# Kernel tuning notes

Measured on AMD Instinct MI355X. Metric: run time of the kernel, lower is better.

The kernel has to match this reference:

```python
import jax, jax.numpy as jnp
import numpy as np
from jax import lax

NUM_CLASSES = 21
KSIZE = 11
DIL = 1
BLUR = 4
NUM_STEPS = 5
YX_SCALE = 80.0
RGB_SCALE = 13.0
POS_SCALE = 3.0


def _ceil_pad_factor(sizes, factor):
    offs = tuple((factor - s % factor) % factor for s in sizes)
    return tuple((o + 1) // 2 for o in offs)


def avg_pool_nopad(x, k, pad):
    # F.avg_pool2d(kernel=stride=k, padding=pad, count_include_pad=False)
    pcfg = ((0, 0), (0, 0), (pad[0], pad[0]), (pad[1], pad[1]))
    s = lax.reduce_window(x, jnp.float32(0), lax.add, (1, 1, k, k), (1, 1, k, k), pcfg)
    ones = jnp.ones((1, 1) + x.shape[2:], x.dtype)
    cnt = lax.reduce_window(ones, jnp.float32(0), lax.add, (1, 1, k, k), (1, 1, k, k), pcfg)
    return s / cnt


def _patches(x, k, dil):
    # im2col with zero padding (matches torch F.unfold used by pac)
    pad = (k // 2) * dil
    p = lax.conv_general_dilated_patches(
        x, (k, k), (1, 1), [(pad, pad), (pad, pad)], rhs_dilation=(dil, dil))
    B, C, H, W = x.shape
    return p.reshape(B, C, k * k, H, W)


def gaussian_kernel(feat, k, dil):
    # pixel-adaptive Gaussian kernel: exp(-0.5 * ||f_i - f_j||^2) over the KxK window
    p = _patches(feat, k, dil)                       # [B,F,k2,H,W]
    d = p - feat[:, :, None]
    return jnp.exp(-0.5 * jnp.sum(d * d, axis=1))    # [B,k2,H,W]


def pac_message(Q, kernel, k, dil):
    # shared-filter (Potts, spatial_filter=False) pac conv: per-channel kernel-weighted sum
    p = _patches(Q, k, dil)                          # [B,C,k2,h,w]
    return jnp.einsum('bckhw,bkhw->bchw', p, kernel)


def upsample_bilinear(x, scale):
    # matches F.interpolate(mode='bilinear', align_corners=False)
    B, C, h, w = x.shape
    def idx_w(n_in):
        n_out = n_in * scale
        src = jnp.clip((jnp.arange(n_out, dtype=jnp.float32) + 0.5) / scale - 0.5, 0.0, n_in - 1.0)
        i0 = jnp.floor(src).astype(jnp.int32)
        i1 = jnp.minimum(i0 + 1, n_in - 1)
        return i0, i1, (src - i0).astype(x.dtype)
    y0, y1, wy = idx_w(h)
    x0, x1, wx = idx_w(w)
    xh = x[:, :, y0, :] * (1 - wy)[None, None, :, None] + x[:, :, y1, :] * wy[None, None, :, None]
    return xh[:, :, :, x0] * (1 - wx)[None, None, None, :] + xh[:, :, :, x1] * wx[None, None, None, :]


def crf_forward(x, w_backbone, b_backbone, unary_weight, pairwise_weights):
    B, _, H, W = x.shape
    # backbone stub: 3x3 conv producing unary logits [B,21,H,W]
    unary = lax.conv_general_dilated(
        x, w_backbone, (1, 1), [(1, 1), (1, 1)],
        dimension_numbers=('NCHW', 'OIHW', 'NCHW')) + b_backbone[None, :, None, None]
    # edge features: bilateral (YX/80, RGB/13) and spatial (YX/3)
    yx = jnp.stack(jnp.meshgrid(jnp.arange(H, dtype=x.dtype), jnp.arange(W, dtype=x.dtype), indexing='ij'))
    yx = jnp.broadcast_to(yx[None], (B, 2, H, W))
    feat_bilateral = jnp.concatenate([yx / YX_SCALE, x / RGB_SCALE], axis=1)  # [B,5,H,W]
    feat_spatial = yx / POS_SCALE                                             # [B,2,H,W]
    pad = _ceil_pad_factor((H, W), BLUR)
    kernels = [gaussian_kernel(avg_pool_nopad(f, BLUR, pad), KSIZE, DIL)
               for f in (feat_bilateral, feat_spatial)]

    def step(logQ, unary, k1, k2, uw, pw):
        Q = jax.nn.softmax(logQ, axis=1)
        Qb = avg_pool_nopad(Q, BLUR, pad)
        new = uw * unary
        for kern, w in ((k1, pw[0]), (k2, pw[1])):
            msg = pac_message(Qb, kern, KSIZE, DIL)
            msg = upsample_bilinear(msg, BLUR)[:, :, pad[0]:pad[0] + H, pad[1]:pad[1] + W]
            new = new + w * msg
        return new

    logQ = unary
    for _ in range(NUM_STEPS):
        logQ = step(logQ, unary, kernels[0], kernels[1], unary_weight, pairwise_weights)
    return logQ  # final_output == 'log_Q'


def setup_inputs():
    key = jax.random.key(0)
    ks = jax.random.split(key, 3)
    B, H, W = 2, 512, 512
    x = jax.random.uniform(ks[0], (B, 3, H, W), jnp.float32) * 255.0  # image in [0,255]
    w_backbone = jax.random.normal(ks[1], (NUM_CLASSES, 3, 3, 3), jnp.float32) * 0.1
    b_backbone = jax.random.normal(ks[2], (NUM_CLASSES,), jnp.float32) * 0.01
    unary_weight = jnp.asarray(0.8, jnp.float32)
    pairwise_weights = jnp.asarray([2.0, 0.6], jnp.float32)
    return {"x": x, "w_backbone": w_backbone, "b_backbone": b_backbone,
            "unary_weight": unary_weight, "pairwise_weights": pairwise_weights}


def reference(x, w_backbone, b_backbone, unary_weight, pairwise_weights):
    return crf_forward(x, w_backbone, b_backbone, unary_weight, pairwise_weights)
```

## Files before the change

### kernel.cpp

```cpp
#include <hip/hip_runtime.h>

#define NCH 21
#define HWP (1 << 14)
#define KS 11
#define KK 121
#define PTW 32
#define PTH 8
#define LROW 48
#define LHGT 18
#define LPLANE (LROW * LHGT)

__global__ __launch_bounds__(256) void k_conv_sm(const float* __restrict__ x,
                                                 const float* __restrict__ w,
                                                 const float* __restrict__ bias,
                                                 float* __restrict__ unary,
                                                 float* __restrict__ qb) {
    int idx = blockIdx.x * 256 + threadIdx.x;
    int r = idx & 3;
    int xqi = (idx >> 2) & 127;
    int py = (idx >> 9) & 127;
    int b = idx >> 16;
    int y = 4 * py + r;
    int xq = xqi << 2;

    float p[3][3][6];
#pragma unroll
    for (int ch = 0; ch < 3; ++ch) {
        const float* xp = x + (((size_t)(b * 3 + ch)) << 18);
#pragma unroll
        for (int rr = 0; rr < 3; ++rr) {
            int yy = y + rr - 1;
            if ((unsigned)yy >= 512u) {
#pragma unroll
                for (int j = 0; j < 6; ++j) p[ch][rr][j] = 0.f;
            } else {
                const float* row = xp + (yy << 9);
                float4 v = *(const float4*)(row + xq);
                p[ch][rr][1] = v.x; p[ch][rr][2] = v.y; p[ch][rr][3] = v.z; p[ch][rr][4] = v.w;
                p[ch][rr][0] = (xq > 0) ? row[xq - 1] : 0.f;
                p[ch][rr][5] = (xq + 4 < 512) ? row[xq + 4] : 0.f;
            }
        }
    }
    float a[NCH][4];
    for (int o = 0; o < NCH; ++o) {
        const float* wp = w + o * 27;
        float bz = bias[o];
        float a0 = bz, a1 = bz, a2 = bz, a3 = bz;
#pragma unroll
        for (int ch = 0; ch < 3; ++ch)
#pragma unroll
            for (int rr = 0; rr < 3; ++rr) {
                float w0 = wp[ch * 9 + rr * 3 + 0];
                float w1 = wp[ch * 9 + rr * 3 + 1];
                float w2 = wp[ch * 9 + rr * 3 + 2];
                const float* pr = p[ch][rr];
                a0 += w0 * pr[0] + w1 * pr[1] + w2 * pr[2];
                a1 += w0 * pr[1] + w1 * pr[2] + w2 * pr[3];
                a2 += w0 * pr[2] + w1 * pr[3] + w2 * pr[4];
                a3 += w0 * pr[3] + w1 * pr[4] + w2 * pr[5];
            }
        *(float4*)(unary + (((size_t)(b * NCH + o)) << 18) + (y << 9) + xq) =
            make_float4(a0, a1, a2, a3);
        a[o][0] = a0; a[o][1] = a1; a[o][2] = a2; a[o][3] = a3;
    }
    float qsum[NCH];
#pragma unroll
    for (int c = 0; c < NCH; ++c) qsum[c] = 0.f;
#pragma unroll
    for (int i2 = 0; i2 < 4; ++i2) {
        float m = a[0][i2];
#pragma unroll
        for (int c = 1; c < NCH; ++c) m = fmaxf(m, a[c][i2]);
        float s = 0.f;
#pragma unroll
        for (int c = 0; c < NCH; ++c) { float e = __expf(a[c][i2] - m); a[c][i2] = e; s += e; }
        float inv = 1.0f / s;
#pragma unroll
        for (int c = 0; c < NCH; ++c) qsum[c] += a[c][i2] * inv;
    }
#pragma unroll
    for (int c = 0; c < NCH; ++c) {
        float v = qsum[c];
        v += __shfl_xor(v, 1);
        v += __shfl_xor(v, 2);
        if (r == 0) qb[(((size_t)(b * NCH + c)) << 14) + (py << 7) + xqi] = v * 0.0625f;
    }
}

__global__ __launch_bounds__(256) void k_pool_rgb(const float* __restrict__ x,
                                                  float* __restrict__ prgb) {
    int idx = blockIdx.x * 256 + threadIdx.x;
    int p = idx & (HWP - 1);
    int ch = (idx >> 14) % 3;
    int b = idx / (3 * HWP);
    int py = p >> 7, px = p & 127;
    const float* xp = x + (((size_t)(b * 3 + ch)) << 18);
    float s = 0.f;
#pragma unroll
    for (int r = 0; r < 4; ++r) {
        const float4 v = *(const float4*)(xp + (((4 * py + r) << 9) + 4 * px));
        s += v.x + v.y + v.z + v.w;
    }
    prgb[idx] = s * 0.0625f;
}

__global__ __launch_bounds__(256) void k_build_kc(const float* __restrict__ prgb,
                                                  const float* __restrict__ pw,
                                                  float* __restrict__ kc) {
    int idx = blockIdx.x * 256 + threadIdx.x;
    int p = idx & (HWP - 1);
    int jj = idx >> 14;
    int b = (jj >= KK) ? 1 : 0;
    int j = jj - KK * b;
    int dy = j / KS, dx = j - dy * KS;
    int py = p >> 7, px = p & 127;
    float pw0 = pw[0], pw1 = pw[1];

    const float inv13 = 1.0f / 13.0f;
    float fy = (4.f * py + 1.5f) * (1.0f / 80.0f);
    float fx = (4.f * px + 1.5f) * (1.0f / 80.0f);
    const float* pb = prgb + (size_t)b * 3 * HWP;
    float r0 = pb[p] * inv13;
    float g0 = pb[HWP + p] * inv13;
    float b0 = pb[2 * HWP + p] * inv13;
    float sy = (4.f * py + 1.5f) * (1.0f / 3.0f);
    float sx = (4.f * px + 1.5f) * (1.0f / 3.0f);

    int ny = py + dy - 5;
    int nx = px + dx - 5;
    float s1, s2;
    if ((unsigned)ny < 128u && (unsigned)nx < 128u) {
        int np = (ny << 7) + nx;
        float r2 = pb[np] * inv13;
        float g2 = pb[HWP + np] * inv13;
        float b2 = pb[2 * HWP + np] * inv13;
        float dya = fy - (4.f * ny + 1.5f) * (1.0f / 80.0f);
        float dxa = fx - (4.f * nx + 1.5f) * (1.0f / 80.0f);
        float dr = r0 - r2, dg = g0 - g2, db = b0 - b2;
        s1 = dya * dya + dxa * dxa + dr * dr + dg * dg + db * db;
        float dys = sy - (4.f * ny + 1.5f) * (1.0f / 3.0f);
        float dxs = sx - (4.f * nx + 1.5f) * (1.0f / 3.0f);
        s2 = dys * dys + dxs * dxs;
    } else {
        s1 = fy * fy + fx * fx + r0 * r0 + g0 * g0 + b0 * b0;
        s2 = sy * sy + sx * sx;
    }
    kc[idx] = pw0 * __expf(-0.5f * s1) + pw1 * __expf(-0.5f * s2);
}

__global__ __launch_bounds__(256) void k_pac4(const float* __restrict__ qb,
                                              const float* __restrict__ kc,
                                              float* __restrict__ msgc) {
    int tile = blockIdx.x & 63;
    int cg = (blockIdx.x >> 6) % 6;
    int b = blockIdx.x / 384;
    int tx0 = (tile & 3) * PTW;
    int ty0 = (tile >> 2) * PTH;
    int c0 = cg * 4;

    __shared__ float lq[4 * LPLANE];

    const float* qbb = qb + (((size_t)(b * NCH)) << 14);
    for (int i = threadIdx.x; i < 4 * LPLANE; i += 256) {
        int c = i / LPLANE;
        int rem = i - c * LPLANE;
        int ly = rem / LROW;
        int lx = rem - ly * LROW;
        int ch = c0 + c;
        int gy = ty0 + ly - 5, gx = tx0 + lx - 5;
        float v = 0.f;
        if (ch < NCH && lx < 42 && (unsigned)gy < 128u && (unsigned)gx < 128u)
            v = qbb[((size_t)ch << 14) + (gy << 7) + gx];
        lq[i] = v;
    }
    __syncthreads();

    int s = threadIdx.x & 63;
    int cl = threadIdx.x >> 6;
    int my = s >> 3;
    int mx0 = (s & 7) << 2;
    int ch = c0 + cl;

    float acc0 = 0.f, acc1 = 0.f, acc2 = 0.f, acc3 = 0.f;
    int p0 = ((ty0 + my) << 7) + tx0 + mx0;
    const float* kcb = kc + (((size_t)(b * KK)) << 14) + p0;
    const float* lbase = lq + cl * LPLANE + mx0;

    for (int dy = 0; dy < KS; ++dy) {
        const float* lp = lbase + (my + dy) * LROW;
        float4 v0 = *(const float4*)(lp + 0);
        float4 v1 = *(const float4*)(lp + 4);
        float4 v2 = *(const float4*)(lp + 8);
        float4 v3 = *(const float4*)(lp + 12);
        float rb[16] = {v0.x, v0.y, v0.z, v0.w, v1.x, v1.y, v1.z, v1.w,
                        v2.x, v2.y, v2.z, v2.w, v3.x, v3.y, v3.z, v3.w};
        const float* kcrow = kcb + (((size_t)(dy * KS)) << 14);
#pragma unroll
        for (int dx = 0; dx < KS; ++dx) {
            float4 k4 = *(const float4*)(kcrow + (((size_t)dx) << 14));
            acc0 += k4.x * rb[dx + 0];
            acc1 += k4.y * rb[dx + 1];
            acc2 += k4.z * rb[dx + 2];
            acc3 += k4.w * rb[dx + 3];
        }
    }
    if (ch < NCH)
        *(float4*)(msgc + (((size_t)(b * NCH + ch)) << 14) + p0) =
            make_float4(acc0, acc1, acc2, acc3);
}

__global__ __launch_bounds__(256) void k_step(const float* __restrict__ unary,
                                              const float* __restrict__ msgc,
                                              const float* __restrict__ uwp,
                                              float* __restrict__ qb,
                                              float* __restrict__ out,
                                              int write_out) {
    int idx = blockIdx.x * 256 + threadIdx.x;
    int r = idx & 3;
    int px = (idx >> 2) & 127;
    int py = (idx >> 9) & 127;
    int b = idx >> 16;
    int y = 4 * py + r;
    float uw = uwp[0];

    int rA = (r < 2) ? max(py - 1, 0) : py;
    int rB = (r < 2) ? py : min(py + 1, 127);
    float fy = (r == 0) ? 0.625f : (r == 1) ? 0.875f : (r == 2) ? 0.125f : 0.375f;
    int xm1 = max(px - 1, 0), xp1 = min(px + 1, 127);
    int oA = rA << 7, oB = rB << 7;

    size_t base = (((size_t)(b * NCH)) << 18) + (y << 9) + (px << 2);
    const float* up = unary + base;
    const float* mp = msgc + (((size_t)(b * NCH)) << 14);

    float a[NCH][4];
#pragma unroll
    for (int c = 0; c < NCH; ++c) {
        float4 u4 = *(const float4*)(up + ((size_t)c << 18));
        const float* m0 = mp + ((size_t)c << 14);
        float aL = m0[oA + xm1], aM = m0[oA + px], aR = m0[oA + xp1];
        float bL = m0[oB + xm1], bM = m0[oB + px], bR = m0[oB + xp1];
        float cL = aL + (bL - aL) * fy;
        float cM = aM + (bM - aM) * fy;
        float cR = aR + (bR - aR) * fy;
        a[c][0] = uw * u4.x + cL + (cM - cL) * 0.625f;
        a[c][1] = uw * u4.y + cL + (cM - cL) * 0.875f;
        a[c][2] = uw * u4.z + cM + (cR - cM) * 0.125f;
        a[c][3] = uw * u4.w + cM + (cR - cM) * 0.375f;
    }

    if (write_out) {
        float* op = out + base;
#pragma unroll
        for (int c = 0; c < NCH; ++c)
            *(float4*)(op + ((size_t)c << 18)) = make_float4(a[c][0], a[c][1], a[c][2], a[c][3]);
        return;
    }

    float qsum[NCH];
#pragma unroll
    for (int c = 0; c < NCH; ++c) qsum[c] = 0.f;
#pragma unroll
    for (int i2 = 0; i2 < 4; ++i2) {
        float m = a[0][i2];
#pragma unroll
        for (int c = 1; c < NCH; ++c) m = fmaxf(m, a[c][i2]);
        float ss = 0.f;
#pragma unroll
        for (int c = 0; c < NCH; ++c) { float e = __expf(a[c][i2] - m); a[c][i2] = e; ss += e; }
        float inv = 1.0f / ss;
#pragma unroll
        for (int c = 0; c < NCH; ++c) qsum[c] += a[c][i2] * inv;
    }
#pragma unroll
    for (int c = 0; c < NCH; ++c) {
        float v = qsum[c];
        v += __shfl_xor(v, 1);
        v += __shfl_xor(v, 2);
        if (r == 0) qb[(((size_t)(b * NCH + c)) << 14) + (py << 7) + px] = v * 0.0625f;
    }
}

extern "C" void kernel_launch(void* const* d_in, const int* in_sizes, int n_in,
                              void* d_out, int out_size, void* d_ws, size_t ws_size,
                              hipStream_t stream) {
    const float* x  = (const float*)d_in[0];
    const float* wb = (const float*)d_in[1];
    const float* bb = (const float*)d_in[2];
    const float* uw = (const float*)d_in[3];
    const float* pw = (const float*)d_in[4];
    float* out = (float*)d_out;

    float* ws    = (float*)d_ws;
    float* unary = ws;
    float* kc    = unary + 11010048;
    float* qb    = kc + 3964928;
    float* msgc  = qb + 688128;
    float* prgb  = msgc;

    k_conv_sm<<<512, 256, 0, stream>>>(x, wb, bb, unary, qb);
    k_pool_rgb<<<384, 256, 0, stream>>>(x, prgb);
    k_build_kc<<<15488, 256, 0, stream>>>(prgb, pw, kc);

    for (int s = 0; s < 5; ++s) {
        k_pac4<<<768, 256, 0, stream>>>(qb, kc, msgc);
        k_step<<<512, 256, 0, stream>>>(unary, msgc, uw, qb, out, (s == 4) ? 1 : 0);
    }
}
```

Baseline: 284.0 us.

## Store PAC kernel weights in fp16 and stage message tile in LDS for step

The precomputed 121-tap Gaussian kernel is stored as half precision, which halves the bytes k_pac4 streams from global memory in each of the five iterations; accumulation stays in fp32. k_step is also reorganised so that each block handles half of one low-res row and first stages the needed three message rows (with clamped halo) into shared memory. The bilinear reads then come from LDS instead of scattered global loads. The cost is reduced kernel-weight precision, which may change outputs slightly, plus an extra barrier and LDS staging in k_step.

```diff
diff --git a/kernel.cpp b/kernel.cpp
--- a/kernel.cpp
+++ b/kernel.cpp
@@ -9,6 +9,8 @@
 #define LROW 48
 #define LHGT 18
 #define LPLANE (LROW * LHGT)
+
+typedef _Float16 half4 __attribute__((ext_vector_type(4)));
 
 __global__ __launch_bounds__(256) void k_conv_sm(const float* __restrict__ x,
                                                  const float* __restrict__ w,
@@ -107,7 +109,7 @@
 
 __global__ __launch_bounds__(256) void k_build_kc(const float* __restrict__ prgb,
                                                   const float* __restrict__ pw,
-                                                  float* __restrict__ kc) {
+                                                  _Float16* __restrict__ kc) {
     int idx = blockIdx.x * 256 + threadIdx.x;
     int p = idx & (HWP - 1);
     int jj = idx >> 14;
@@ -146,11 +148,11 @@
         s1 = fy * fy + fx * fx + r0 * r0 + g0 * g0 + b0 * b0;
         s2 = sy * sy + sx * sx;
     }
-    kc[idx] = pw0 * __expf(-0.5f * s1) + pw1 * __expf(-0.5f * s2);
+    kc[idx] = (_Float16)(pw0 * __expf(-0.5f * s1) + pw1 * __expf(-0.5f * s2));
 }
 
 __global__ __launch_bounds__(256) void k_pac4(const float* __restrict__ qb,
-                                              const float* __restrict__ kc,
+                                              const _Float16* __restrict__ kc,
                                               float* __restrict__ msgc) {
     int tile = blockIdx.x & 63;
     int cg = (blockIdx.x >> 6) % 6;
@@ -184,7 +186,7 @@
 
     float acc0 = 0.f, acc1 = 0.f, acc2 = 0.f, acc3 = 0.f;
     int p0 = ((ty0 + my) << 7) + tx0 + mx0;
-    const float* kcb = kc + (((size_t)(b * KK)) << 14) + p0;
+    const _Float16* kcb = kc + (((size_t)(b * KK)) << 14) + p0;
     const float* lbase = lq + cl * LPLANE + mx0;
 
     for (int dy = 0; dy < KS; ++dy) {
@@ -195,14 +197,14 @@
         float4 v3 = *(const float4*)(lp + 12);
         float rb[16] = {v0.x, v0.y, v0.z, v0.w, v1.x, v1.y, v1.z, v1.w,
                         v2.x, v2.y, v2.z, v2.w, v3.x, v3.y, v3.z, v3.w};
-        const float* kcrow = kcb + (((size_t)(dy * KS)) << 14);
+        const _Float16* kcrow = kcb + (((size_t)(dy * KS)) << 14);
 #pragma unroll
         for (int dx = 0; dx < KS; ++dx) {
-            float4 k4 = *(const float4*)(kcrow + (((size_t)dx) << 14));
-            acc0 += k4.x * rb[dx + 0];
-            acc1 += k4.y * rb[dx + 1];
-            acc2 += k4.z * rb[dx + 2];
-            acc3 += k4.w * rb[dx + 3];
+            half4 k4 = *(const half4*)(kcrow + (((size_t)dx) << 14));
+            acc0 += (float)k4.x * rb[dx + 0];
+            acc1 += (float)k4.y * rb[dx + 1];
+            acc2 += (float)k4.z * rb[dx + 2];
+            acc3 += (float)k4.w * rb[dx + 3];
         }
     }
     if (ch < NCH)
@@ -216,31 +218,46 @@
                                               float* __restrict__ qb,
                                               float* __restrict__ out,
                                               int write_out) {
-    int idx = blockIdx.x * 256 + threadIdx.x;
-    int r = idx & 3;
-    int px = (idx >> 2) & 127;
-    int py = (idx >> 9) & 127;
-    int b = idx >> 16;
+    int half = blockIdx.x & 1;
+    int py = (blockIdx.x >> 1) & 127;
+    int b = blockIdx.x >> 8;
+    int px0 = half << 6;
+
+    __shared__ float lmsg[NCH * 3 * 66];
+
+    const float* mbase = msgc + (((size_t)(b * NCH)) << 14);
+    for (int i = threadIdx.x; i < NCH * 198; i += 256) {
+        int c = i / 198;
+        int rem = i - c * 198;
+        int row = rem / 66;
+        int j = rem - row * 66;
+        int ry = min(max(py - 1 + row, 0), 127);
+        int gx = min(max(px0 - 1 + j, 0), 127);
+        lmsg[i] = mbase[((size_t)c << 14) + (ry << 7) + gx];
+    }
+    __syncthreads();
+
+    int r = threadIdx.x & 3;
+    int lpx = threadIdx.x >> 2;
+    int px = px0 + lpx;
     int y = 4 * py + r;
     float uw = uwp[0];
 
-    int rA = (r < 2) ? max(py - 1, 0) : py;
-    int rB = (r < 2) ? py : min(py + 1, 127);
+    int iA = (r < 2) ? 0 : 1;
+    int iB = iA + 1;
     float fy = (r == 0) ? 0.625f : (r == 1) ? 0.875f : (r == 2) ? 0.125f : 0.375f;
-    int xm1 = max(px - 1, 0), xp1 = min(px + 1, 127);
-    int oA = rA << 7, oB = rB << 7;
 
     size_t base = (((size_t)(b * NCH)) << 18) + (y << 9) + (px << 2);
     const float* up = unary + base;
-    const float* mp = msgc + (((size_t)(b * NCH)) << 14);
 
     float a[NCH][4];
 #pragma unroll
     for (int c = 0; c < NCH; ++c) {
         float4 u4 = *(const float4*)(up + ((size_t)c << 18));
-        const float* m0 = mp + ((size_t)c << 14);
-        float aL = m0[oA + xm1], aM = m0[oA + px], aR = m0[oA + xp1];
-        float bL = m0[oB + xm1], bM = m0[oB + px], bR = m0[oB + xp1];
+        const float* lA = lmsg + c * 198 + iA * 66 + lpx;
+        const float* lB = lmsg + c * 198 + iB * 66 + lpx;
+        float aL = lA[0], aM = lA[1], aR = lA[2];
+        float bL = lB[0], bM = lB[1], bR = lB[2];
         float cL = aL + (bL - aL) * fy;
         float cM = aM + (bM - aM) * fy;
         float cR = aR + (bR - aR) * fy;
@@ -294,8 +311,8 @@
 
     float* ws    = (float*)d_ws;
     float* unary = ws;
-    float* kc    = unary + 11010048;
-    float* qb    = kc + 3964928;
+    _Float16* kc = (_Float16*)(unary + 11010048);
+    float* qb    = (float*)(kc + 3964928);
     float* msgc  = qb + 688128;
     float* prgb  = msgc;
 
```

New measurement: 272.9 us. 3.9% less time.
